# Kernel optimization log

Measured on AMD Instinct MI355X. Metric: run time of the kernel, lower is better.

The kernel has to match this reference:

```python
import jax, jax.numpy as jnp
import numpy as np
import math

HIDDEN_DIM = 1024
NUM_HEADS = 16
HEAD_DIM = HIDDEN_DIM // NUM_HEADS  # 64

def setup_inputs() -> dict:
    key = jax.random.key(0)
    k1, k2, k3 = jax.random.split(key, 3)
    x = jax.random.normal(k1, (8, 4096, HIDDEN_DIM), dtype=jnp.float32)
    W = jax.random.normal(k2, (HIDDEN_DIM, NUM_HEADS), dtype=jnp.float32) * (1.0 / math.sqrt(HIDDEN_DIM))
    mask = jax.random.randint(k3, (8, 4096), 0, 2, dtype=jnp.int32)
    return {"x": x, "W": W, "mask": mask}

def reference(x, W, mask):
    B, S, D = x.shape
    # linear scoring: [B,S,H], scaled by sqrt(head_dim)
    logits = jnp.einsum('bsd,dh->bsh', x, W) / math.sqrt(HEAD_DIM)
    # mask out padded positions (mask==0 -> -inf) before softmax over seq axis
    logits = jnp.where(mask[:, :, None] == 0, -jnp.inf, logits)
    attn = jax.nn.softmax(logits, axis=1)  # softmax over sequence dim
    # dropout is identity in eval mode
    # weighted sum: original expands x over heads, so each head pools the full hidden vector
    pooled = jnp.einsum('bsh,bsd->bhd', attn, x)  # [B, H, D]
    return pooled.reshape(B, NUM_HEADS * D)
```

## Files before the change

### kernel.cpp

```cpp
#include <hip/hip_runtime.h>
#include <math.h>

#define BB 8
#define SS 4096
#define DD 1024
#define HH 16

typedef __attribute__((ext_vector_type(4))) float f32x4;
typedef __fp16 fp16x2 __attribute__((ext_vector_type(2)));
typedef _Float16 half8v __attribute__((ext_vector_type(8)));


__global__ __launch_bounds__(256) void k_prepw(
    const float* __restrict__ W, ushort* __restrict__ wh16, ushort* __restrict__ wl16) {
  int i = blockIdx.x * 256 + threadIdx.x;
  int t = i >> 9;
  int l = (i >> 3) & 63;
  int e = i & 7;
  int d = t * 32 + (l >> 4) * 8 + e;
  int h = l & 15;
  float w = W[d * HH + h];
  _Float16 wh = (_Float16)w;
  _Float16 wl = (_Float16)(w - (float)wh);
  union { _Float16 f; ushort u; } ch, cl;
  ch.f = wh; cl.f = wl;
  wh16[i] = ch.u;
  wl16[i] = cl.u;
}

__global__ __launch_bounds__(256, 4) void k_logits(
    const float* __restrict__ x, const ushort* __restrict__ wh16,
    const ushort* __restrict__ wl16, float* __restrict__ plog) {
  __shared__ float4 lds4[2][4][16][16];

  const int tid = threadIdx.x;
  const int lane = tid & 63;
  const int wv = tid >> 6;
  const int kh = blockIdx.x & 1;
  const int tile = blockIdx.x >> 1;
  const int b = tile >> 6;
  const int s0 = (tile & 63) * 64;
  const int r15 = lane & 15;
  const int kg = lane >> 4;
  const int srow = lane >> 4;
  const int sul = lane & 15;

  const float* xw = x + ((size_t)b * SS + s0 + wv * 16) * DD + kh * 512;
  const half8v* bhp = reinterpret_cast<const half8v*>(wh16) + (kh * 16 * 64 + lane);
  const half8v* blp = reinterpret_cast<const half8v*>(wl16) + (kh * 16 * 64 + lane);

  f32x4 acch = {0.f, 0.f, 0.f, 0.f};
  f32x4 accl = {0.f, 0.f, 0.f, 0.f};

  float4 st[4];
#pragma unroll
  for (int k = 0; k < 4; ++k) {
    int row = k * 4 + srow;
    st[k] = *reinterpret_cast<const float4*>(xw + (size_t)row * DD + sul * 4);
  }
#pragma unroll
  for (int k = 0; k < 4; ++k) {
    int row = k * 4 + srow;
    lds4[0][wv][row][sul ^ (row & 7)] = st[k];
  }

#pragma unroll
  for (int c = 0; c < 8; ++c) {
    if (c < 7) {
#pragma unroll
      for (int k = 0; k < 4; ++k) {
        int row = k * 4 + srow;
        st[k] = *reinterpret_cast<const float4*>(
            xw + (size_t)row * DD + (c + 1) * 64 + sul * 4);
      }
    }

#pragma unroll
    for (int t4 = 0; t4 < 2; ++t4) {
      const int t = c * 2 + t4;
      half8v bh = bhp[t * 64];
      half8v bl = blp[t * 64];
      const int u0 = t4 * 8 + kg * 2;
      float4 va = lds4[c & 1][wv][r15][u0 ^ (r15 & 7)];
      float4 vb = lds4[c & 1][wv][r15][(u0 + 1) ^ (r15 & 7)];
      union { fp16x2 h2[4]; half8v h8; } ax;
      ax.h2[0] = __builtin_amdgcn_cvt_pkrtz(va.x, va.y);
      ax.h2[1] = __builtin_amdgcn_cvt_pkrtz(va.z, va.w);
      ax.h2[2] = __builtin_amdgcn_cvt_pkrtz(vb.x, vb.y);
      ax.h2[3] = __builtin_amdgcn_cvt_pkrtz(vb.z, vb.w);
      acch = __builtin_amdgcn_mfma_f32_16x16x32_f16(ax.h8, bh, acch, 0, 0, 0);
      accl = __builtin_amdgcn_mfma_f32_16x16x32_f16(ax.h8, bl, accl, 0, 0, 0);
    }

    if (c < 7) {
#pragma unroll
      for (int k = 0; k < 4; ++k) {
        int row = k * 4 + srow;
        lds4[(c + 1) & 1][wv][row][sul ^ (row & 7)] = st[k];
      }
    }
  }

  float* ob = plog + (size_t)kh * (BB * SS * HH) +
              ((size_t)b * SS + s0 + wv * 16) * HH;
#pragma unroll
  for (int q = 0; q < 4; ++q)
    ob[(size_t)(kg * 4 + q) * HH + r15] = acch[q] + accl[q];
}

__device__ __forceinline__ float wave_max64(float v) {
#pragma unroll
  for (int off = 32; off > 0; off >>= 1) v = fmaxf(v, __shfl_xor(v, off, 64));
  return v;
}
__device__ __forceinline__ float wave_sum64(float v) {
#pragma unroll
  for (int off = 32; off > 0; off >>= 1) v += __shfl_xor(v, off, 64);
  return v;
}

__global__ __launch_bounds__(256) void k_softmax(
    const float* __restrict__ plog, const int* __restrict__ mask,
    float* __restrict__ wout) {
  __shared__ float sred[4];
  const int tid = threadIdx.x;
  const int lane = tid & 63;
  const int wv = tid >> 6;
  const int b = blockIdx.x >> 4;
  const int h = blockIdx.x & 15;
  const float* b0 = plog + (size_t)b * SS * HH + h;
  const float* b1 = b0 + (size_t)BB * SS * HH;
  const int* mb = mask + b * SS;

  float v[16];
  float m = -INFINITY;
#pragma unroll
  for (int k = 0; k < 16; ++k) {
    int s = k * 256 + tid;
    float lv = (b0[(size_t)s * HH] + b1[(size_t)s * HH]) * 0.125f;
    v[k] = mb[s] ? lv : -INFINITY;
    m = fmaxf(m, v[k]);
  }
  m = wave_max64(m);
  if (lane == 0) sred[wv] = m;
  __syncthreads();
  m = fmaxf(fmaxf(sred[0], sred[1]), fmaxf(sred[2], sred[3]));
  __syncthreads();

  float ssum = 0.f;
#pragma unroll
  for (int k = 0; k < 16; ++k) {
    v[k] = __expf(v[k] - m);
    ssum += v[k];
  }
  ssum = wave_sum64(ssum);
  if (lane == 0) sred[wv] = ssum;
  __syncthreads();
  float inv = 1.0f / (sred[0] + sred[1] + sred[2] + sred[3]);
#pragma unroll
  for (int k = 0; k < 16; ++k) {
    int s = k * 256 + tid;
    wout[((size_t)b * SS + s) * HH + h] = v[k] * inv;
  }
}

__global__ __launch_bounds__(256) void k_pool(
    const float* __restrict__ x, const float* __restrict__ wn,
    float* __restrict__ partial) {
  __shared__ float wl[128][16];
  const int tid = threadIdx.x;
  const int dh = blockIdx.x & 1;
  const int sc = (blockIdx.x >> 1) & 31;
  const int b = blockIdx.x >> 6;
  const int s0 = sc * 128;

#pragma unroll
  for (int k = 0; k < 2; ++k) {
    int f = k * 256 + tid;
    float4 v = *reinterpret_cast<const float4*>(wn + ((size_t)b * SS + s0) * HH + f * 4);
    *reinterpret_cast<float4*>(&wl[0][0] + f * 4) = v;
  }
  __syncthreads();

  float2 acc[HH];
#pragma unroll
  for (int h = 0; h < HH; ++h) acc[h] = make_float2(0.f, 0.f);

  const float* xb = x + ((size_t)b * SS + s0) * DD + dh * 512 + tid * 2;
  for (int s = 0; s < 128; ++s) {
    float2 xv = *reinterpret_cast<const float2*>(xb + (size_t)s * DD);
    const float4* wrow = reinterpret_cast<const float4*>(wl[s]);
    float4 wa = wrow[0], wb_ = wrow[1], wc = wrow[2], wd = wrow[3];
    float wvv[16] = {wa.x, wa.y, wa.z, wa.w, wb_.x, wb_.y, wb_.z, wb_.w,
                     wc.x, wc.y, wc.z, wc.w, wd.x, wd.y, wd.z, wd.w};
#pragma unroll
    for (int h = 0; h < HH; ++h) {
      float w = wvv[h];
      acc[h].x += w * xv.x;
      acc[h].y += w * xv.y;
    }
  }

  float* pb = partial + ((size_t)sc * BB + b) * (HH * DD) + dh * 512 + tid * 2;
#pragma unroll
  for (int h = 0; h < HH; ++h)
    *reinterpret_cast<float2*>(pb + (size_t)h * DD) = acc[h];
}

__global__ __launch_bounds__(256) void k_reduce(
    const float* __restrict__ partial, float* __restrict__ out) {
  const int idx = blockIdx.x * 256 + threadIdx.x;
  float s = 0.f;
#pragma unroll
  for (int c = 0; c < 32; ++c) s += partial[(size_t)c * (BB * HH * DD) + idx];
  out[idx] = s;
}

extern "C" void kernel_launch(void* const* d_in, const int* in_sizes, int n_in,
                              void* d_out, int out_size, void* d_ws, size_t ws_size,
                              hipStream_t stream) {
  const float* x = (const float*)d_in[0];
  const float* W = (const float*)d_in[1];
  const int* mask = (const int*)d_in[2];
  float* out = (float*)d_out;

  char* ws = (char*)d_ws;
  float* plog    = (float*)ws;
  float* wbuf    = (float*)(ws + (size_t)4 * 1024 * 1024);
  float* partial = (float*)(ws + (size_t)6 * 1024 * 1024);
  ushort* wh16   = (ushort*)(ws + (size_t)22 * 1024 * 1024);
  ushort* wl16   = (ushort*)(ws + (size_t)22 * 1024 * 1024 + 32 * 1024);

  k_prepw<<<64, 256, 0, stream>>>(W, wh16, wl16);
  k_logits<<<1024, 256, 0, stream>>>(x, wh16, wl16, plog);
  k_softmax<<<128, 256, 0, stream>>>(plog, mask, wbuf);
  k_pool<<<512, 256, 0, stream>>>(x, wbuf, partial);
  k_reduce<<<512, 256, 0, stream>>>(partial, out);
}
```

Baseline: 80.50 us.

## Split softmax into chunked online max/sum partials and fuse normalization into pool

The monolithic per-(batch,head) softmax kernel, which read strided logits and wrote a normalized weight buffer, is replaced. A new kernel computes per-128-row chunk running max and sum using online-softmax merging with coalesced float4 reads. The pool kernel now merges the 32 chunk partials itself and recomputes exp-normalized weights directly from the logits, removing the weight buffer round trip. Separately, the logits kernel gets deeper register double-buffering of x loads and prefetches the fp16 W fragments one step ahead, at the cost of more registers under a 4-wave occupancy bound.

```diff
diff --git a/kernel.cpp b/kernel.cpp
--- a/kernel.cpp
+++ b/kernel.cpp
@@ -10,6 +10,13 @@
 typedef __fp16 fp16x2 __attribute__((ext_vector_type(2)));
 typedef _Float16 half8v __attribute__((ext_vector_type(8)));
 
+
+__device__ __forceinline__ void sm_merge(float& m, float& z, float om, float oz) {
+  float nm = fmaxf(m, om);
+  if (nm > -INFINITY)
+    z = z * __expf(m - nm) + oz * __expf(om - nm);
+  m = nm;
+}
 
 __global__ __launch_bounds__(256) void k_prepw(
     const float* __restrict__ W, ushort* __restrict__ wh16, ushort* __restrict__ wl16) {
@@ -52,34 +59,48 @@
   f32x4 acch = {0.f, 0.f, 0.f, 0.f};
   f32x4 accl = {0.f, 0.f, 0.f, 0.f};
 
-  float4 st[4];
+  float4 stA[4], stB[4];
+  half8v whc[2], wlc[2], whn[2], wln[2];
+
 #pragma unroll
   for (int k = 0; k < 4; ++k) {
     int row = k * 4 + srow;
-    st[k] = *reinterpret_cast<const float4*>(xw + (size_t)row * DD + sul * 4);
-  }
+    stA[k] = *reinterpret_cast<const float4*>(xw + (size_t)row * DD + sul * 4);
+  }
+#pragma unroll
+  for (int j = 0; j < 2; ++j) { whc[j] = bhp[j * 64]; wlc[j] = blp[j * 64]; }
 #pragma unroll
   for (int k = 0; k < 4; ++k) {
     int row = k * 4 + srow;
-    lds4[0][wv][row][sul ^ (row & 7)] = st[k];
+    lds4[0][wv][row][sul ^ (row & 7)] = stA[k];
+  }
+#pragma unroll
+  for (int k = 0; k < 4; ++k) {
+    int row = k * 4 + srow;
+    stB[k] = *reinterpret_cast<const float4*>(xw + (size_t)row * DD + 64 + sul * 4);
   }
 
 #pragma unroll
   for (int c = 0; c < 8; ++c) {
-    if (c < 7) {
+    if (c < 6) {
+      float4* stN = ((c & 1) == 0) ? stA : stB;
 #pragma unroll
       for (int k = 0; k < 4; ++k) {
         int row = k * 4 + srow;
-        st[k] = *reinterpret_cast<const float4*>(
-            xw + (size_t)row * DD + (c + 1) * 64 + sul * 4);
+        stN[k] = *reinterpret_cast<const float4*>(
+            xw + (size_t)row * DD + (c + 2) * 64 + sul * 4);
       }
     }
+    if (c < 7) {
+#pragma unroll
+      for (int j = 0; j < 2; ++j) {
+        whn[j] = bhp[((c + 1) * 2 + j) * 64];
+        wln[j] = blp[((c + 1) * 2 + j) * 64];
+      }
+    }
 
 #pragma unroll
     for (int t4 = 0; t4 < 2; ++t4) {
-      const int t = c * 2 + t4;
-      half8v bh = bhp[t * 64];
-      half8v bl = blp[t * 64];
       const int u0 = t4 * 8 + kg * 2;
       float4 va = lds4[c & 1][wv][r15][u0 ^ (r15 & 7)];
       float4 vb = lds4[c & 1][wv][r15][(u0 + 1) ^ (r15 & 7)];
@@ -88,16 +109,19 @@
       ax.h2[1] = __builtin_amdgcn_cvt_pkrtz(va.z, va.w);
       ax.h2[2] = __builtin_amdgcn_cvt_pkrtz(vb.x, vb.y);
       ax.h2[3] = __builtin_amdgcn_cvt_pkrtz(vb.z, vb.w);
-      acch = __builtin_amdgcn_mfma_f32_16x16x32_f16(ax.h8, bh, acch, 0, 0, 0);
-      accl = __builtin_amdgcn_mfma_f32_16x16x32_f16(ax.h8, bl, accl, 0, 0, 0);
+      acch = __builtin_amdgcn_mfma_f32_16x16x32_f16(ax.h8, whc[t4], acch, 0, 0, 0);
+      accl = __builtin_amdgcn_mfma_f32_16x16x32_f16(ax.h8, wlc[t4], accl, 0, 0, 0);
     }
 
     if (c < 7) {
+      float4* stW = (((c + 1) & 1) == 0) ? stA : stB;
 #pragma unroll
       for (int k = 0; k < 4; ++k) {
         int row = k * 4 + srow;
-        lds4[(c + 1) & 1][wv][row][sul ^ (row & 7)] = st[k];
+        lds4[(c + 1) & 1][wv][row][sul ^ (row & 7)] = stW[k];
       }
+      whc[0] = whn[0]; whc[1] = whn[1];
+      wlc[0] = wln[0]; wlc[1] = wln[1];
     }
   }
 
@@ -108,77 +132,110 @@
     ob[(size_t)(kg * 4 + q) * HH + r15] = acch[q] + accl[q];
 }
 
-__device__ __forceinline__ float wave_max64(float v) {
-#pragma unroll
-  for (int off = 32; off > 0; off >>= 1) v = fmaxf(v, __shfl_xor(v, off, 64));
-  return v;
-}
-__device__ __forceinline__ float wave_sum64(float v) {
-#pragma unroll
-  for (int off = 32; off > 0; off >>= 1) v += __shfl_xor(v, off, 64);
-  return v;
-}
-
-__global__ __launch_bounds__(256) void k_softmax(
+__global__ __launch_bounds__(256) void k_smpart(
     const float* __restrict__ plog, const int* __restrict__ mask,
-    float* __restrict__ wout) {
-  __shared__ float sred[4];
+    float2* __restrict__ bred) {
+  __shared__ float4 smm[4][4], smz[4][4];
   const int tid = threadIdx.x;
   const int lane = tid & 63;
   const int wv = tid >> 6;
-  const int b = blockIdx.x >> 4;
-  const int h = blockIdx.x & 15;
-  const float* b0 = plog + (size_t)b * SS * HH + h;
-  const float* b1 = b0 + (size_t)BB * SS * HH;
-  const int* mb = mask + b * SS;
-
-  float v[16];
-  float m = -INFINITY;
-#pragma unroll
-  for (int k = 0; k < 16; ++k) {
-    int s = k * 256 + tid;
-    float lv = (b0[(size_t)s * HH] + b1[(size_t)s * HH]) * 0.125f;
-    v[k] = mb[s] ? lv : -INFINITY;
-    m = fmaxf(m, v[k]);
-  }
-  m = wave_max64(m);
-  if (lane == 0) sred[wv] = m;
+  const int b = blockIdx.x >> 5;
+  const int sc = blockIdx.x & 31;
+  const int s0 = sc * 128;
+  const float4* p0 = reinterpret_cast<const float4*>(plog + ((size_t)b * SS + s0) * HH);
+  const float4* p1 = reinterpret_cast<const float4*>(
+      plog + (size_t)BB * SS * HH + ((size_t)b * SS + s0) * HH);
+  const int* mb = mask + b * SS + s0;
+
+  float m4[4] = {-INFINITY, -INFINITY, -INFINITY, -INFINITY};
+  float z4[4] = {0.f, 0.f, 0.f, 0.f};
+#pragma unroll
+  for (int i = 0; i < 2; ++i) {
+    int f = i * 256 + tid;
+    float4 va = p0[f];
+    float4 vb = p1[f];
+    int msk = mb[f >> 2];
+    float lv[4] = {(va.x + vb.x) * 0.125f, (va.y + vb.y) * 0.125f,
+                   (va.z + vb.z) * 0.125f, (va.w + vb.w) * 0.125f};
+#pragma unroll
+    for (int j = 0; j < 4; ++j) {
+      float v = msk ? lv[j] : -INFINITY;
+      sm_merge(m4[j], z4[j], v, 1.0f);
+    }
+  }
+#pragma unroll
+  for (int off = 4; off < 64; off <<= 1) {
+#pragma unroll
+    for (int j = 0; j < 4; ++j) {
+      float om = __shfl_xor(m4[j], off, 64);
+      float oz = __shfl_xor(z4[j], off, 64);
+      sm_merge(m4[j], z4[j], om, oz);
+    }
+  }
+  if (lane < 4) {
+    smm[wv][lane] = make_float4(m4[0], m4[1], m4[2], m4[3]);
+    smz[wv][lane] = make_float4(z4[0], z4[1], z4[2], z4[3]);
+  }
   __syncthreads();
-  m = fmaxf(fmaxf(sred[0], sred[1]), fmaxf(sred[2], sred[3]));
-  __syncthreads();
-
-  float ssum = 0.f;
-#pragma unroll
-  for (int k = 0; k < 16; ++k) {
-    v[k] = __expf(v[k] - m);
-    ssum += v[k];
-  }
-  ssum = wave_sum64(ssum);
-  if (lane == 0) sred[wv] = ssum;
-  __syncthreads();
-  float inv = 1.0f / (sred[0] + sred[1] + sred[2] + sred[3]);
-#pragma unroll
-  for (int k = 0; k < 16; ++k) {
-    int s = k * 256 + tid;
-    wout[((size_t)b * SS + s) * HH + h] = v[k] * inv;
+  if (tid < 4) {
+    float4 mm = smm[0][tid], zz = smz[0][tid];
+    float fm[4] = {mm.x, mm.y, mm.z, mm.w};
+    float fz[4] = {zz.x, zz.y, zz.z, zz.w};
+#pragma unroll
+    for (int w = 1; w < 4; ++w) {
+      float4 om4 = smm[w][tid], oz4 = smz[w][tid];
+      float om[4] = {om4.x, om4.y, om4.z, om4.w};
+      float oz[4] = {oz4.x, oz4.y, oz4.z, oz4.w};
+#pragma unroll
+      for (int j = 0; j < 4; ++j) sm_merge(fm[j], fz[j], om[j], oz[j]);
+    }
+#pragma unroll
+    for (int j = 0; j < 4; ++j)
+      bred[((size_t)b * 32 + sc) * HH + tid * 4 + j] = make_float2(fm[j], fz[j]);
   }
 }
 
 __global__ __launch_bounds__(256) void k_pool(
-    const float* __restrict__ x, const float* __restrict__ wn,
+    const float* __restrict__ x, const float* __restrict__ plog,
+    const float2* __restrict__ bred, const int* __restrict__ mask,
     float* __restrict__ partial) {
   __shared__ float wl[128][16];
+  __shared__ float fm[16], fz[16];
   const int tid = threadIdx.x;
   const int dh = blockIdx.x & 1;
   const int sc = (blockIdx.x >> 1) & 31;
   const int b = blockIdx.x >> 6;
   const int s0 = sc * 128;
 
+  if (tid < 16) {
+    float m = -INFINITY, z = 0.f;
+#pragma unroll 4
+    for (int c = 0; c < 32; ++c) {
+      float2 p = bred[((size_t)b * 32 + c) * HH + tid];
+      sm_merge(m, z, p.x, p.y);
+    }
+    fm[tid] = m;
+    fz[tid] = (z > 0.f) ? 1.0f / z : 0.f;
+  }
+  __syncthreads();
+
+  const float4* p0 = reinterpret_cast<const float4*>(plog + ((size_t)b * SS + s0) * HH);
+  const float4* p1 = reinterpret_cast<const float4*>(
+      plog + (size_t)BB * SS * HH + ((size_t)b * SS + s0) * HH);
+  const int* mb = mask + b * SS + s0;
 #pragma unroll
   for (int k = 0; k < 2; ++k) {
     int f = k * 256 + tid;
-    float4 v = *reinterpret_cast<const float4*>(wn + ((size_t)b * SS + s0) * HH + f * 4);
-    *reinterpret_cast<float4*>(&wl[0][0] + f * 4) = v;
+    float4 va = p0[f];
+    float4 vb = p1[f];
+    int msk = mb[f >> 2];
+    int hb = (f & 3) * 4;
+    float4 w;
+    w.x = msk ? __expf((va.x + vb.x) * 0.125f - fm[hb + 0]) * fz[hb + 0] : 0.f;
+    w.y = msk ? __expf((va.y + vb.y) * 0.125f - fm[hb + 1]) * fz[hb + 1] : 0.f;
+    w.z = msk ? __expf((va.z + vb.z) * 0.125f - fm[hb + 2]) * fz[hb + 2] : 0.f;
+    w.w = msk ? __expf((va.w + vb.w) * 0.125f - fm[hb + 3]) * fz[hb + 3] : 0.f;
+    *reinterpret_cast<float4*>(&wl[0][0] + f * 4) = w;
   }
   __syncthreads();
 
@@ -226,14 +283,14 @@
 
   char* ws = (char*)d_ws;
   float* plog    = (float*)ws;
-  float* wbuf    = (float*)(ws + (size_t)4 * 1024 * 1024);
   float* partial = (float*)(ws + (size_t)6 * 1024 * 1024);
   ushort* wh16   = (ushort*)(ws + (size_t)22 * 1024 * 1024);
   ushort* wl16   = (ushort*)(ws + (size_t)22 * 1024 * 1024 + 32 * 1024);
+  float2* bred   = (float2*)(ws + (size_t)23 * 1024 * 1024);
 
   k_prepw<<<64, 256, 0, stream>>>(W, wh16, wl16);
   k_logits<<<1024, 256, 0, stream>>>(x, wh16, wl16, plog);
-  k_softmax<<<128, 256, 0, stream>>>(plog, mask, wbuf);
-  k_pool<<<512, 256, 0, stream>>>(x, wbuf, partial);
+  k_smpart<<<256, 256, 0, stream>>>(plog, mask, bred);
+  k_pool<<<512, 256, 0, stream>>>(x, plog, bred, mask, partial);
   k_reduce<<<512, 256, 0, stream>>>(partial, out);
 }
```

Measured after the change: 74.96 us. -6.9%, faster.

## Fuse softmax into logits and pool via online max/sum partials

Applied to the files above, without the earlier changes.

Removes the separate softmax kernel. The logits kernel now applies the mask and scale, writes masked logits, and emits per-tile (max, sum-exp) partials merged with an online-softmax combine. The pool kernel merges the 64 partials per batch, then computes normalized weights on the fly. The logits kernel also stops splitting K across two blocks, which drops the two-way logit sum. It gains a deeper three-stage x prefetch with double-buffered W fragments and drops launch bounds to 2 waves per SIMD. This cuts one launch and a pass over the logits but halves the grid, and every pool block redundantly merges 64 partials.

```diff
diff --git a/kernel.cpp b/kernel.cpp
--- a/kernel.cpp
+++ b/kernel.cpp
@@ -10,6 +10,13 @@
 typedef __fp16 fp16x2 __attribute__((ext_vector_type(2)));
 typedef _Float16 half8v __attribute__((ext_vector_type(8)));
 
+
+__device__ __forceinline__ void sm_merge(float& m, float& z, float om, float oz) {
+  float nm = fmaxf(m, om);
+  if (nm > -INFINITY)
+    z = z * __expf(m - nm) + oz * __expf(om - nm);
+  m = nm;
+}
 
 __global__ __launch_bounds__(256) void k_prepw(
     const float* __restrict__ W, ushort* __restrict__ wh16, ushort* __restrict__ wl16) {
@@ -28,58 +35,63 @@
   wl16[i] = cl.u;
 }
 
-__global__ __launch_bounds__(256, 4) void k_logits(
+#define XLOAD(dst, c)                                                          \
+  _Pragma("unroll") for (int k = 0; k < 4; ++k) {                              \
+    int row = k * 4 + srow;                                                    \
+    dst[k] = *reinterpret_cast<const float4*>(                                 \
+        xw + (size_t)row * DD + (c) * 64 + sul * 4);                           \
+  }
+#define XSTAGE(src, c)                                                         \
+  _Pragma("unroll") for (int k = 0; k < 4; ++k) {                              \
+    int row = k * 4 + srow;                                                    \
+    lds4[(c) & 1][wv][row][sul ^ (row & 7)] = src[k];                          \
+  }
+#define WLOAD(c)                                                               \
+  whf[(c) & 1][0] = bhp[(2 * (c) + 0) * 64];                                   \
+  whf[(c) & 1][1] = bhp[(2 * (c) + 1) * 64];                                   \
+  wlf[(c) & 1][0] = blp[(2 * (c) + 0) * 64];                                   \
+  wlf[(c) & 1][1] = blp[(2 * (c) + 1) * 64];
+
+__global__ __launch_bounds__(256, 2) void k_logits(
     const float* __restrict__ x, const ushort* __restrict__ wh16,
-    const ushort* __restrict__ wl16, float* __restrict__ plog) {
+    const ushort* __restrict__ wl16, const int* __restrict__ mask,
+    float* __restrict__ plog, float2* __restrict__ bred) {
   __shared__ float4 lds4[2][4][16][16];
+  __shared__ float2 smch[4][16];
 
   const int tid = threadIdx.x;
   const int lane = tid & 63;
-  const int wv = tid >> 6;
-  const int kh = blockIdx.x & 1;
-  const int tile = blockIdx.x >> 1;
-  const int b = tile >> 6;
-  const int s0 = (tile & 63) * 64;
+  const int wv = __builtin_amdgcn_readfirstlane(tid >> 6);
+  const int b = blockIdx.x >> 6;
+  const int tile = blockIdx.x & 63;
+  const int s0 = tile * 64;
   const int r15 = lane & 15;
   const int kg = lane >> 4;
   const int srow = lane >> 4;
   const int sul = lane & 15;
 
-  const float* xw = x + ((size_t)b * SS + s0 + wv * 16) * DD + kh * 512;
-  const half8v* bhp = reinterpret_cast<const half8v*>(wh16) + (kh * 16 * 64 + lane);
-  const half8v* blp = reinterpret_cast<const half8v*>(wl16) + (kh * 16 * 64 + lane);
+  const float* xw = x + ((size_t)b * SS + s0 + wv * 16) * DD;
+  const half8v* bhp = reinterpret_cast<const half8v*>(wh16) + lane;
+  const half8v* blp = reinterpret_cast<const half8v*>(wl16) + lane;
 
   f32x4 acch = {0.f, 0.f, 0.f, 0.f};
   f32x4 accl = {0.f, 0.f, 0.f, 0.f};
-
-  float4 st[4];
-#pragma unroll
-  for (int k = 0; k < 4; ++k) {
-    int row = k * 4 + srow;
-    st[k] = *reinterpret_cast<const float4*>(xw + (size_t)row * DD + sul * 4);
-  }
-#pragma unroll
-  for (int k = 0; k < 4; ++k) {
-    int row = k * 4 + srow;
-    lds4[0][wv][row][sul ^ (row & 7)] = st[k];
-  }
-
-#pragma unroll
-  for (int c = 0; c < 8; ++c) {
-    if (c < 7) {
-#pragma unroll
-      for (int k = 0; k < 4; ++k) {
-        int row = k * 4 + srow;
-        st[k] = *reinterpret_cast<const float4*>(
-            xw + (size_t)row * DD + (c + 1) * 64 + sul * 4);
-      }
-    }
+  float4 st[3][4];
+  half8v whf[2][2], wlf[2][2];
+
+  XLOAD(st[0], 0);
+  XLOAD(st[1], 1);
+  XLOAD(st[2], 2);
+  XSTAGE(st[0], 0);
+  WLOAD(0);
+  WLOAD(1);
+
+#pragma unroll
+  for (int c = 0; c < 16; ++c) {
+    if (c < 13) { XLOAD(st[(c + 3) % 3], c + 3); }
 
 #pragma unroll
     for (int t4 = 0; t4 < 2; ++t4) {
-      const int t = c * 2 + t4;
-      half8v bh = bhp[t * 64];
-      half8v bl = blp[t * 64];
       const int u0 = t4 * 8 + kg * 2;
       float4 va = lds4[c & 1][wv][r15][u0 ^ (r15 & 7)];
       float4 vb = lds4[c & 1][wv][r15][(u0 + 1) ^ (r15 & 7)];
@@ -88,97 +100,88 @@
       ax.h2[1] = __builtin_amdgcn_cvt_pkrtz(va.z, va.w);
       ax.h2[2] = __builtin_amdgcn_cvt_pkrtz(vb.x, vb.y);
       ax.h2[3] = __builtin_amdgcn_cvt_pkrtz(vb.z, vb.w);
-      acch = __builtin_amdgcn_mfma_f32_16x16x32_f16(ax.h8, bh, acch, 0, 0, 0);
-      accl = __builtin_amdgcn_mfma_f32_16x16x32_f16(ax.h8, bl, accl, 0, 0, 0);
-    }
-
-    if (c < 7) {
-#pragma unroll
-      for (int k = 0; k < 4; ++k) {
-        int row = k * 4 + srow;
-        lds4[(c + 1) & 1][wv][row][sul ^ (row & 7)] = st[k];
-      }
-    }
-  }
-
-  float* ob = plog + (size_t)kh * (BB * SS * HH) +
-              ((size_t)b * SS + s0 + wv * 16) * HH;
-#pragma unroll
-  for (int q = 0; q < 4; ++q)
-    ob[(size_t)(kg * 4 + q) * HH + r15] = acch[q] + accl[q];
-}
-
-__device__ __forceinline__ float wave_max64(float v) {
-#pragma unroll
-  for (int off = 32; off > 0; off >>= 1) v = fmaxf(v, __shfl_xor(v, off, 64));
-  return v;
-}
-__device__ __forceinline__ float wave_sum64(float v) {
-#pragma unroll
-  for (int off = 32; off > 0; off >>= 1) v += __shfl_xor(v, off, 64);
-  return v;
-}
-
-__global__ __launch_bounds__(256) void k_softmax(
-    const float* __restrict__ plog, const int* __restrict__ mask,
-    float* __restrict__ wout) {
-  __shared__ float sred[4];
-  const int tid = threadIdx.x;
-  const int lane = tid & 63;
-  const int wv = tid >> 6;
-  const int b = blockIdx.x >> 4;
-  const int h = blockIdx.x & 15;
-  const float* b0 = plog + (size_t)b * SS * HH + h;
-  const float* b1 = b0 + (size_t)BB * SS * HH;
-  const int* mb = mask + b * SS;
-
-  float v[16];
-  float m = -INFINITY;
-#pragma unroll
-  for (int k = 0; k < 16; ++k) {
-    int s = k * 256 + tid;
-    float lv = (b0[(size_t)s * HH] + b1[(size_t)s * HH]) * 0.125f;
-    v[k] = mb[s] ? lv : -INFINITY;
-    m = fmaxf(m, v[k]);
-  }
-  m = wave_max64(m);
-  if (lane == 0) sred[wv] = m;
+      acch = __builtin_amdgcn_mfma_f32_16x16x32_f16(ax.h8, whf[c & 1][t4], acch, 0, 0, 0);
+      accl = __builtin_amdgcn_mfma_f32_16x16x32_f16(ax.h8, wlf[c & 1][t4], accl, 0, 0, 0);
+    }
+
+    if (c < 14) { WLOAD(c + 2); }
+    if (c < 15) { XSTAGE(st[(c + 1) % 3], c + 1); }
+  }
+
+  float lv[4];
+  float* ob = plog + ((size_t)b * SS + s0 + wv * 16) * HH;
+#pragma unroll
+  for (int q = 0; q < 4; ++q) {
+    int srw = kg * 4 + q;
+    int msk = mask[b * SS + s0 + wv * 16 + srw];
+    float v = (acch[q] + accl[q]) * 0.125f;
+    lv[q] = msk ? v : -INFINITY;
+    ob[(size_t)srw * HH + r15] = lv[q];
+  }
+  float ml = fmaxf(fmaxf(lv[0], lv[1]), fmaxf(lv[2], lv[3]));
+  float zl = 0.f;
+  if (ml > -INFINITY) {
+#pragma unroll
+    for (int q = 0; q < 4; ++q) zl += __expf(lv[q] - ml);
+  }
+#pragma unroll
+  for (int off = 16; off < 64; off <<= 1) {
+    float om = __shfl_xor(ml, off, 64);
+    float oz = __shfl_xor(zl, off, 64);
+    sm_merge(ml, zl, om, oz);
+  }
+  if (kg == 0) smch[wv][r15] = make_float2(ml, zl);
   __syncthreads();
-  m = fmaxf(fmaxf(sred[0], sred[1]), fmaxf(sred[2], sred[3]));
-  __syncthreads();
-
-  float ssum = 0.f;
-#pragma unroll
-  for (int k = 0; k < 16; ++k) {
-    v[k] = __expf(v[k] - m);
-    ssum += v[k];
-  }
-  ssum = wave_sum64(ssum);
-  if (lane == 0) sred[wv] = ssum;
-  __syncthreads();
-  float inv = 1.0f / (sred[0] + sred[1] + sred[2] + sred[3]);
-#pragma unroll
-  for (int k = 0; k < 16; ++k) {
-    int s = k * 256 + tid;
-    wout[((size_t)b * SS + s) * HH + h] = v[k] * inv;
+  if (tid < 16) {
+    float2 p0 = smch[0][tid];
+    float m = p0.x, z = p0.y;
+#pragma unroll
+    for (int w = 1; w < 4; ++w) {
+      float2 pw = smch[w][tid];
+      sm_merge(m, z, pw.x, pw.y);
+    }
+    bred[((size_t)b * 64 + tile) * HH + tid] = make_float2(m, z);
   }
 }
 
 __global__ __launch_bounds__(256) void k_pool(
-    const float* __restrict__ x, const float* __restrict__ wn,
+    const float* __restrict__ x, const float* __restrict__ plog,
+    const float2* __restrict__ bred, const int* __restrict__ mask,
     float* __restrict__ partial) {
   __shared__ float wl[128][16];
+  __shared__ float fm[16], fz[16];
   const int tid = threadIdx.x;
   const int dh = blockIdx.x & 1;
   const int sc = (blockIdx.x >> 1) & 31;
   const int b = blockIdx.x >> 6;
   const int s0 = sc * 128;
 
+  if (tid < 16) {
+    float m = -INFINITY, z = 0.f;
+#pragma unroll 4
+    for (int c = 0; c < 64; ++c) {
+      float2 p = bred[((size_t)b * 64 + c) * HH + tid];
+      sm_merge(m, z, p.x, p.y);
+    }
+    fm[tid] = m;
+    fz[tid] = (z > 0.f) ? 1.0f / z : 0.f;
+  }
+  __syncthreads();
+
+  const float4* p0 = reinterpret_cast<const float4*>(plog + ((size_t)b * SS + s0) * HH);
+  const int* mb = mask + b * SS + s0;
 #pragma unroll
   for (int k = 0; k < 2; ++k) {
     int f = k * 256 + tid;
-    float4 v = *reinterpret_cast<const float4*>(wn + ((size_t)b * SS + s0) * HH + f * 4);
-    *reinterpret_cast<float4*>(&wl[0][0] + f * 4) = v;
+    float4 va = p0[f];
+    int msk = mb[f >> 2];
+    int hb = (f & 3) * 4;
+    float4 w;
+    w.x = msk ? __expf(va.x - fm[hb + 0]) * fz[hb + 0] : 0.f;
+    w.y = msk ? __expf(va.y - fm[hb + 1]) * fz[hb + 1] : 0.f;
+    w.z = msk ? __expf(va.z - fm[hb + 2]) * fz[hb + 2] : 0.f;
+    w.w = msk ? __expf(va.w - fm[hb + 3]) * fz[hb + 3] : 0.f;
+    *reinterpret_cast<float4*>(&wl[0][0] + f * 4) = w;
   }
   __syncthreads();
 
@@ -226,14 +229,13 @@
 
   char* ws = (char*)d_ws;
   float* plog    = (float*)ws;
-  float* wbuf    = (float*)(ws + (size_t)4 * 1024 * 1024);
   float* partial = (float*)(ws + (size_t)6 * 1024 * 1024);
   ushort* wh16   = (ushort*)(ws + (size_t)22 * 1024 * 1024);
   ushort* wl16   = (ushort*)(ws + (size_t)22 * 1024 * 1024 + 32 * 1024);
+  float2* bred   = (float2*)(ws + (size_t)23 * 1024 * 1024);
 
   k_prepw<<<64, 256, 0, stream>>>(W, wh16, wl16);
-  k_logits<<<1024, 256, 0, stream>>>(x, wh16, wl16, plog);
-  k_softmax<<<128, 256, 0, stream>>>(plog, mask, wbuf);
-  k_pool<<<512, 256, 0, stream>>>(x, wbuf, partial);
+  k_logits<<<512, 256, 0, stream>>>(x, wh16, wl16, mask, plog, bred);
+  k_pool<<<512, 256, 0, stream>>>(x, plog, bred, mask, partial);
   k_reduce<<<512, 256, 0, stream>>>(partial, out);
 }
```

After: 70.99 us. -11.8%, faster.
